# Optimization experiments

Hardware: AMD Instinct MI355X
Metric: run time of the kernel (lower is better)

## Reference

```python
import jax, jax.numpy as jnp
import numpy as np
import math

EMBED_DIM = 1024
NUM_HEADS = 16
HEAD_DIM = EMBED_DIM // NUM_HEADS
ROPE_BASE = 10000.0


def _rope_cache(seq_len, dim, dtype=jnp.float32):
    inv_freq = 1.0 / (ROPE_BASE ** (jnp.arange(0, dim, 2, dtype=jnp.float32) / dim))
    t = jnp.arange(seq_len, dtype=jnp.float32)
    freqs = t[:, None] * inv_freq[None, :]          # [S, D/2]
    emb = jnp.concatenate([freqs, freqs], axis=-1)  # [S, D]
    return jnp.cos(emb).astype(dtype), jnp.sin(emb).astype(dtype)


def _rotate_half(x):
    x1, x2 = jnp.split(x, 2, axis=-1)
    return jnp.concatenate([-x2, x1], axis=-1)


def setup_inputs() -> dict:
    key = jax.random.key(0)
    ks = jax.random.split(key, 12)
    B, S, E = 2, 2048, EMBED_DIM
    s = 1.0 / math.sqrt(E)
    inp = {
        "query": jax.random.normal(ks[0], (B, S, E), jnp.float32),
        "key": jax.random.normal(ks[1], (B, S, E), jnp.float32),
        "value": jax.random.normal(ks[2], (B, S, E), jnp.float32),
        "Wq": jax.random.normal(ks[3], (E, E), jnp.float32) * s,
        "bq": jnp.zeros((E,), jnp.float32),
        "Wk": jax.random.normal(ks[4], (E, E), jnp.float32) * s,
        "bk": jnp.zeros((E,), jnp.float32),
        "Wv": jax.random.normal(ks[5], (E, E), jnp.float32) * s,
        "bv": jnp.zeros((E,), jnp.float32),
        "Wo": jax.random.normal(ks[6], (E, E), jnp.float32) * s,
        "bo": jnp.zeros((E,), jnp.float32),
    }
    return inp


def reference(query, key, value, Wq, bq, Wk, bk, Wv, bv, Wo, bo):
    B, S, E = query.shape
    H, D = NUM_HEADS, HEAD_DIM

    def proj(x, W, b):  # torch Linear: x @ W.T + b -> [B,H,S,D]
        return (x @ W.T + b).reshape(B, -1, H, D).transpose(0, 2, 1, 3)

    q = proj(query, Wq, bq)
    k = proj(key, Wk, bk)
    v = proj(value, Wv, bv)

    cos, sin = _rope_cache(S, D, q.dtype)  # [S, D]
    cos = cos[None, None]                  # [1,1,S,D]
    sin = sin[None, None]
    q = q * cos + _rotate_half(q) * sin
    k = k * cos + _rotate_half(k) * sin

    scale = 1.0 / math.sqrt(D)
    scores = jnp.einsum("bhsd,bhtd->bhst", q, k) * scale  # [B,H,S,S]
    causal = jnp.triu(jnp.ones((S, S), bool), k=1)
    scores = jnp.where(causal[None, None], -jnp.inf, scores)
    attn = jax.nn.softmax(scores, axis=-1)
    out = jnp.einsum("bhst,bhtd->bhsd", attn, v)           # [B,H,S,D]
    out = out.transpose(0, 2, 1, 3).reshape(B, S, E)
    return out @ Wo.T + bo
```

## Files before the change

kernel.cpp:

```cpp
#include <hip/hip_runtime.h>
#include <math.h>

typedef unsigned short u16;
typedef __attribute__((ext_vector_type(4))) float f32x4;
typedef __attribute__((ext_vector_type(8))) short bf16x8;

#define SEQ   2048
#define EMB   1024
#define NH    16
#define HD    64
#define MROWS 4096

__device__ __forceinline__ u16 f2b(float f) {
    unsigned u = __float_as_uint(f);
    u += 0x7fff + ((u >> 16) & 1);
    return (u16)(u >> 16);
}
__device__ __forceinline__ unsigned pack_bf16x2(float a, float b) {
    unsigned ua = __float_as_uint(a) + 0x8000u;
    unsigned ub = __float_as_uint(b) + 0x8000u;
    return __builtin_amdgcn_perm(ub, ua, 0x07060302u);
}
__device__ __forceinline__ void gld16(const u16* g, const u16* l) {
    __builtin_amdgcn_global_load_lds((const __attribute__((address_space(1))) void*)g,
                                     (__attribute__((address_space(3))) void*)l, 16, 0, 0);
}

struct F2BArgs { const float* s[7]; u16* d[7]; };

__global__ void k_f2b(F2BArgs a) {
    int id = blockIdx.x;
    const float* src; u16* dst; int base;
    if (id < 6144) {
        int z = id >> 11;
        src = a.s[z]; dst = a.d[z];
        base = (id & 2047) << 8;
    } else {
        int r = id - 6144;
        int z = 3 + (r >> 9);
        src = a.s[z]; dst = a.d[z];
        base = (r & 511) << 8;
    }
    int i = base + threadIdx.x;
    const float4* s4 = (const float4*)src;
    float4 x = s4[i * 2], y = s4[i * 2 + 1];
    union { u16 u[8]; uint4 v; } o;
    o.u[0] = f2b(x.x); o.u[1] = f2b(x.y); o.u[2] = f2b(x.z); o.u[3] = f2b(x.w);
    o.u[4] = f2b(y.x); o.u[5] = f2b(y.y); o.u[6] = f2b(y.z); o.u[7] = f2b(y.w);
    ((uint4*)dst)[i] = o.v;
}

struct GemmArgs {
    const u16* A; const u16* Bw; const float* bias; u16* Cb;
};

__global__ __launch_bounds__(256) void k_gemm_qkv(GemmArgs g0, GemmArgs g1, GemmArgs g2) {
    __shared__ u16 sbuf[2][8192];

    int id = blockIdx.x;
    int x = id / 96;
    int rem = id % 96;
    int z = rem >> 5;
    int y = rem & 31;
    GemmArgs g = (z == 0) ? g0 : (z == 1 ? g1 : g2);

    int tid = threadIdx.x;
    int wave = tid >> 6, lane = tid & 63, quad = lane >> 4, l16 = lane & 15;
    int wm = wave >> 1, wn = wave & 1;
    int m0 = y * 128, n0 = x * 128;
    const int K = EMB;

    auto stage = [&](int k0, u16* buf) {
#pragma unroll
        for (int pp = 0; pp < 4; pp++) {
            int slot = pp * 256 + tid;
            int p = slot & 3;
            const u16* gsrc;
            if (pp < 2) {
                int row = slot >> 2;
                int c = p ^ (row & 3);
                gsrc = g.A + (size_t)(m0 + row) * K + k0 + c * 8;
            } else {
                int row = (slot >> 2) - 128;
                int c = p ^ (row & 3);
                gsrc = g.Bw + (size_t)(n0 + row) * K + k0 + c * 8;
            }
            gld16(gsrc, buf + slot * 8);
        }
    };

    f32x4 acc[4][4];
#pragma unroll
    for (int i = 0; i < 4; i++)
#pragma unroll
        for (int j = 0; j < 4; j++) acc[i][j] = (f32x4){0.f, 0.f, 0.f, 0.f};

    int nk = K >> 5;
    stage(0, sbuf[0]);
    for (int ks = 0; ks < nk; ks++) {
        __syncthreads();
        if (ks + 1 < nk) stage((ks + 1) << 5, sbuf[(ks + 1) & 1]);
        const u16* Ab = sbuf[ks & 1];
        const u16* Bb = Ab + 4096;
        bf16x8 af[4], bfr[4];
#pragma unroll
        for (int i = 0; i < 4; i++) {
            int row = wm * 64 + i * 16 + l16;
            af[i] = *(const bf16x8*)&Ab[row * 32 + (quad ^ (row & 3)) * 8];
        }
#pragma unroll
        for (int j = 0; j < 4; j++) {
            int row = wn * 64 + j * 16 + l16;
            bfr[j] = *(const bf16x8*)&Bb[row * 32 + (quad ^ (row & 3)) * 8];
        }
#pragma unroll
        for (int i = 0; i < 4; i++)
#pragma unroll
            for (int j = 0; j < 4; j++)
                acc[i][j] = __builtin_amdgcn_mfma_f32_16x16x32_bf16(af[i], bfr[j], acc[i][j], 0, 0, 0);
    }

    if (z < 2) {
        float qscale = (z == 0) ? 0.18033688011112042f : 1.0f;
#pragma unroll
        for (int j = 0; j < 2; j++) {
            int col1 = n0 + wn * 64 + j * 16 + l16;
            int dd1 = col1 & 63;
            int h = col1 >> 6;
            float inv = __expf(-(float)dd1 * 0.28782313662425575f);
            float b1 = g.bias[col1], b2 = g.bias[col1 + 32];
#pragma unroll
            for (int i = 0; i < 4; i++)
#pragma unroll
                for (int r = 0; r < 4; r++) {
                    int row = m0 + wm * 64 + i * 16 + quad * 4 + r;
                    int b = row >> 11, s = row & (SEQ - 1);
                    float sn, cs;
                    __sincosf((float)s * inv, &sn, &cs);
                    float x1 = acc[i][j][r] + b1;
                    float x2 = acc[i][j + 2][r] + b2;
                    size_t base = ((size_t)(b * NH + h) * SEQ + s) << 6;
                    g.Cb[base + dd1]      = f2b((x1 * cs - x2 * sn) * qscale);
                    g.Cb[base + dd1 + 32] = f2b((x2 * cs + x1 * sn) * qscale);
                }
        }
    } else {
        __syncthreads();
        u16* tr = &sbuf[0][0] + wave * 4096;
        int h = (n0 >> 6) + wn;
        int b = m0 >> 11;
        int s0 = (m0 & (SEQ - 1)) + wm * 64;
#pragma unroll
        for (int j = 0; j < 4; j++) {
            float bv = g.bias[n0 + wn * 64 + j * 16 + l16];
#pragma unroll
            for (int i = 0; i < 4; i++) {
                uint2 pk;
                pk.x = pack_bf16x2(acc[i][j][0] + bv, acc[i][j][1] + bv);
                pk.y = pack_bf16x2(acc[i][j][2] + bv, acc[i][j][3] + bv);
                int row = j * 16 + l16;
                int c4 = i * 4 + quad;
                *(uint2*)&tr[row * 64 + ((c4 ^ (row & 14)) << 2)] = pk;
            }
        }
        u16* dst = g.Cb + (((size_t)(b * NH + h) * HD) * SEQ) + s0;
#pragma unroll
        for (int ps = 0; ps < 8; ps++) {
            int d = ps * 8 + (lane >> 3);
            int c4 = (lane & 7) * 2;
            uint4 v = *(const uint4*)&tr[d * 64 + ((c4 ^ (d & 14)) << 2)];
            *(uint4*)&dst[(size_t)d * SEQ + c4 * 4] = v;
        }
    }
}

__global__ __launch_bounds__(256) void k_gemm_o(const u16* __restrict__ A,
                                                const u16* __restrict__ Bw,
                                                const float* __restrict__ bias,
                                                float* __restrict__ C) {
    __shared__ u16 sb[2][6144];
    int tid = threadIdx.x;
    int w = tid >> 6, lane = tid & 63, quad = lane >> 4, l16 = lane & 15;
    int y = blockIdx.x & 63, x = blockIdx.x >> 6;
    int m0 = y * 64, n0 = x * 128;
    const int K = EMB;

    auto stage = [&](int k0, u16* buf) {
#pragma unroll
        for (int pp = 0; pp < 3; pp++) {
            int slot = pp * 256 + tid;
            if (slot < 256) {
                int row = slot >> 2, p = slot & 3;
                int c = p ^ (row & 3);
                gld16(A + (size_t)(m0 + row) * K + k0 + c * 8, buf + slot * 8);
            } else {
                int s2 = slot - 256;
                int row = s2 >> 2, p = s2 & 3;
                int c = p ^ (row & 3);
                gld16(Bw + (size_t)(n0 + row) * K + k0 + c * 8, buf + 2048 + s2 * 8);
            }
        }
    };

    f32x4 acc[4][2];
#pragma unroll
    for (int i = 0; i < 4; i++)
#pragma unroll
        for (int j = 0; j < 2; j++) acc[i][j] = (f32x4){0.f, 0.f, 0.f, 0.f};

    int nk = K >> 5;
    stage(0, sb[0]);
    for (int ks = 0; ks < nk; ks++) {
        __syncthreads();
        if (ks + 1 < nk) stage((ks + 1) << 5, sb[(ks + 1) & 1]);
        const u16* Ab = sb[ks & 1];
        const u16* Bb = Ab + 2048;
        bf16x8 af[4], bf[2];
#pragma unroll
        for (int i = 0; i < 4; i++) {
            int row = i * 16 + l16;
            af[i] = *(const bf16x8*)&Ab[row * 32 + (quad ^ (row & 3)) * 8];
        }
#pragma unroll
        for (int j = 0; j < 2; j++) {
            int row = w * 32 + j * 16 + l16;
            bf[j] = *(const bf16x8*)&Bb[row * 32 + (quad ^ (row & 3)) * 8];
        }
#pragma unroll
        for (int i = 0; i < 4; i++)
#pragma unroll
            for (int j = 0; j < 2; j++)
                acc[i][j] = __builtin_amdgcn_mfma_f32_16x16x32_bf16(af[i], bf[j], acc[i][j], 0, 0, 0);
    }

#pragma unroll
    for (int i = 0; i < 4; i++)
#pragma unroll
        for (int r = 0; r < 4; r++) {
            int row = m0 + i * 16 + quad * 4 + r;
#pragma unroll
            for (int j = 0; j < 2; j++) {
                int col = n0 + w * 32 + j * 16 + l16;
                C[(size_t)row * EMB + col] = acc[i][j][r] + bias[col];
            }
        }
}

__global__ __launch_bounds__(512, 2) void k_attn(const u16* __restrict__ Q,
                                                 const u16* __restrict__ K,
                                                 const u16* __restrict__ Vt,
                                                 u16* __restrict__ O) {
    __shared__ u16 kv[4][8192];
    __shared__ u16 Pl[8][1024];
    int tid = threadIdx.x;
    int w = tid >> 6, lane = tid & 63, quad = lane >> 4, l16 = lane & 15;
    int pair = w & 3, par = w >> 2;
    int bh = blockIdx.x & 31;
    int qt = 15 - (blockIdx.x >> 5);
    int q0w = qt * 128 + pair * 32;

    const u16* Qb = Q + (size_t)bh * SEQ * HD;
    const u16* Kb = K + (size_t)bh * SEQ * HD;
    const u16* Vb = Vt + (size_t)bh * HD * SEQ;
    u16* pl = Pl[w];

    auto stage = [&](int t0, u16* buf) {
#pragma unroll
        for (int pp = 0; pp < 2; pp++) {
            int slot = pp * 512 + tid;
            int r = (slot >> 3) & 63;
            int p = slot & 7;
            int c = p ^ (r & 7);
            const u16* gsrc = (pp < 1) ? Kb + (size_t)(t0 + r) * HD + c * 8
                                       : Vb + (size_t)r * SEQ + t0 + c * 8;
            gld16(gsrc, buf + slot * 8);
        }
    };

    bf16x8 bq[2][2];
#pragma unroll
    for (int g = 0; g < 2; g++) {
        size_t base = (size_t)(q0w + g * 16 + l16) * HD + quad * 8;
        bq[g][0] = *(const bf16x8*)&Qb[base];
        bq[g][1] = *(const bf16x8*)&Qb[base + 32];
    }

    f32x4 o2[2][4];
#pragma unroll
    for (int g = 0; g < 2; g++)
#pragma unroll
        for (int jd = 0; jd < 4; jd++) o2[g][jd] = (f32x4){0.f, 0.f, 0.f, 0.f};
    float l_p[2] = {0.f, 0.f};

    int nsup = qt + 1;
    stage(0, kv[0]);
    stage(64, kv[2]);
    for (int k = 0; k < nsup; ++k) {
        __syncthreads();
        if (k + 1 < nsup) {
            stage((k + 1) * 128,      kv[(k + 1) & 1]);
            stage((k + 1) * 128 + 64, kv[2 + ((k + 1) & 1)]);
        }
        int t0 = k * 128 + par * 64;
        if (t0 > q0w + 31) continue;

        const u16* Kl = kv[par * 2 + (k & 1)];
        const u16* Vl = Kl + 4096;

        bf16x8 kf[4][2], vf[4][2];
#pragma unroll
        for (int mt = 0; mt < 4; mt++) {
            int row = mt * 16 + l16;
            kf[mt][0] = *(const bf16x8*)&Kl[row * 64 + (quad ^ (row & 7)) * 8];
            kf[mt][1] = *(const bf16x8*)&Kl[row * 64 + ((quad + 4) ^ (row & 7)) * 8];
            vf[mt][0] = *(const bf16x8*)&Vl[row * 64 + (quad ^ (row & 7)) * 8];
            vf[mt][1] = *(const bf16x8*)&Vl[row * 64 + ((quad + 4) ^ (row & 7)) * 8];
        }

#pragma unroll
        for (int g = 0; g < 2; g++) {
            int qmin = q0w + g * 16;
            if (t0 > qmin + 15) continue;

            f32x4 sc[4];
#pragma unroll
            for (int mt = 0; mt < 4; mt++) {
                sc[mt] = (f32x4){0.f, 0.f, 0.f, 0.f};
                sc[mt] = __builtin_amdgcn_mfma_f32_16x16x32_bf16(kf[mt][0], bq[g][0], sc[mt], 0, 0, 0);
                sc[mt] = __builtin_amdgcn_mfma_f32_16x16x32_bf16(kf[mt][1], bq[g][1], sc[mt], 0, 0, 0);
            }

            if (t0 + 63 > qmin) {
                int q = qmin + l16;
#pragma unroll
                for (int mt = 0; mt < 4; mt++)
#pragma unroll
                    for (int r = 0; r < 4; r++) {
                        int t = t0 + mt * 16 + quad * 4 + r;
                        if (t > q) sc[mt][r] = -INFINITY;
                    }
            }

            float rs = 0.f;
#pragma unroll
            for (int mt = 0; mt < 4; mt++)
#pragma unroll
                for (int r = 0; r < 4; r++) {
                    float p = __builtin_amdgcn_exp2f(sc[mt][r] - 64.f);
                    sc[mt][r] = p;
                    rs += p;
                }
            l_p[g] += rs;

#pragma unroll
            for (int mt = 0; mt < 4; mt++) {
                uint2 pk;
                pk.x = pack_bf16x2(sc[mt][0], sc[mt][1]);
                pk.y = pack_bf16x2(sc[mt][2], sc[mt][3]);
                int chunk = 2 * mt + (quad >> 1);
                *(uint2*)&pl[l16 * 64 + (chunk ^ (l16 & 7)) * 8 + (quad & 1) * 4] = pk;
            }

            bf16x8 pb0 = *(const bf16x8*)&pl[l16 * 64 + (quad ^ (l16 & 7)) * 8];
            bf16x8 pb1 = *(const bf16x8*)&pl[l16 * 64 + ((quad + 4) ^ (l16 & 7)) * 8];

#pragma unroll
            for (int jd = 0; jd < 4; jd++) {
                o2[g][jd] = __builtin_amdgcn_mfma_f32_16x16x32_bf16(vf[jd][0], pb0, o2[g][jd], 0, 0, 0);
                o2[g][jd] = __builtin_amdgcn_mfma_f32_16x16x32_bf16(vf[jd][1], pb1, o2[g][jd], 0, 0, 0);
            }
        }
    }

    __syncthreads();
    float* mp = (float*)&kv[0][0] + pair * 2176;
    if (par) {
#pragma unroll
        for (int g = 0; g < 2; g++) {
#pragma unroll
            for (int jd = 0; jd < 4; jd++)
                *(f32x4*)&mp[(g * 4 + jd) * 256 + lane * 4] = o2[g][jd];
            mp[2048 + g * 64 + lane] = l_p[g];
        }
    }
    __syncthreads();
    if (par) return;
#pragma unroll
    for (int g = 0; g < 2; g++) {
#pragma unroll
        for (int jd = 0; jd < 4; jd++)
            o2[g][jd] += *(const f32x4*)&mp[(g * 4 + jd) * 256 + lane * 4];
        l_p[g] += mp[2048 + g * 64 + lane];
    }

    u16* ep = ((u16*)&kv[0][0]) + 18432 + pair * 1216;
    int b = bh >> 4, h = bh & (NH - 1);
#pragma unroll
    for (int g = 0; g < 2; g++) {
        float l = l_p[g];
        l += __shfl_xor(l, 16, 64);
        l += __shfl_xor(l, 32, 64);
        float inv = 1.f / l;
#pragma unroll
        for (int jd = 0; jd < 4; jd++) {
            uint2 pk;
            pk.x = pack_bf16x2(o2[g][jd][0] * inv, o2[g][jd][1] * inv);
            pk.y = pack_bf16x2(o2[g][jd][2] * inv, o2[g][jd][3] * inv);
            *(uint2*)&ep[l16 * 72 + jd * 16 + quad * 4] = pk;
        }
        int row = lane >> 2, dc = (lane & 3) * 16;
        uint4 d0 = *(const uint4*)&ep[row * 72 + dc];
        uint4 d1 = *(const uint4*)&ep[row * 72 + dc + 8];
        int q = q0w + g * 16 + row;
        size_t addr = (size_t)(b * SEQ + q) * EMB + h * HD + dc;
        *(uint4*)&O[addr] = d0;
        *(uint4*)&O[addr + 8] = d1;
    }
}

extern "C" void kernel_launch(void* const* d_in, const int* in_sizes, int n_in,
                              void* d_out, int out_size, void* d_ws, size_t ws_size,
                              hipStream_t stream) {
    const float* query = (const float*)d_in[0];
    const float* key_  = (const float*)d_in[1];
    const float* value = (const float*)d_in[2];
    const float* Wq = (const float*)d_in[3];
    const float* bq = (const float*)d_in[4];
    const float* Wk = (const float*)d_in[5];
    const float* bk = (const float*)d_in[6];
    const float* Wv = (const float*)d_in[7];
    const float* bv = (const float*)d_in[8];
    const float* Wo = (const float*)d_in[9];
    const float* bo = (const float*)d_in[10];
    float* out = (float*)d_out;

    char* ws = (char*)d_ws;
    const size_t MB = 1u << 20;
    u16* xq  = (u16*)(ws + 0 * MB);
    u16* xk  = (u16*)(ws + 8 * MB);
    u16* xv  = (u16*)(ws + 16 * MB);
    u16* wqb = (u16*)(ws + 24 * MB);
    u16* wkb = (u16*)(ws + 26 * MB);
    u16* wvb = (u16*)(ws + 28 * MB);
    u16* wob = (u16*)(ws + 30 * MB);
    u16* Qp  = (u16*)(ws + 32 * MB);
    u16* Kp  = (u16*)(ws + 40 * MB);
    u16* Vt  = (u16*)(ws + 48 * MB);
    u16* Ab  = xk;

    F2BArgs fa;
    fa.s[0] = query; fa.s[1] = key_; fa.s[2] = value;
    fa.s[3] = Wq; fa.s[4] = Wk; fa.s[5] = Wv; fa.s[6] = Wo;
    fa.d[0] = xq; fa.d[1] = xk; fa.d[2] = xv;
    fa.d[3] = wqb; fa.d[4] = wkb; fa.d[5] = wvb; fa.d[6] = wob;
    k_f2b<<<8192, 256, 0, stream>>>(fa);

    GemmArgs gq = { xq, wqb, bq, Qp };
    GemmArgs gk = { xk, wkb, bk, Kp };
    GemmArgs gv = { xv, wvb, bv, Vt };
    k_gemm_qkv<<<768, 256, 0, stream>>>(gq, gk, gv);

    k_attn<<<512, 512, 0, stream>>>(Qp, Kp, Vt, Ab);

    k_gemm_o<<<512, 256, 0, stream>>>(Ab, wob, bo, out);
}
```

Before: 209.0 us.

## Enlarge QKV GEMM tile to 256x128 with triple-buffered async LDS pipeline

The QKV projection GEMM moves to 512-thread blocks, each computing a 256x128 tile, with a K-step of 64 and three LDS buffers kept two stages ahead. Waits use explicit vmcnt counts instead of __syncthreads, so global-to-LDS loads overlap with MFMA work, and the swizzle widens to 8 chunks for the 64-wide rows. The aim is to cut barrier and latency stalls and improve operand reuse. The cost is 144KB of LDS per block, which limits occupancy, and the hand-written waitcnt logic could be fragile.

```diff
diff --git a/kernel.cpp b/kernel.cpp
--- a/kernel.cpp
+++ b/kernel.cpp
@@ -54,35 +54,35 @@
     const u16* A; const u16* Bw; const float* bias; u16* Cb;
 };
 
-__global__ __launch_bounds__(256) void k_gemm_qkv(GemmArgs g0, GemmArgs g1, GemmArgs g2) {
-    __shared__ u16 sbuf[2][8192];
+__global__ __launch_bounds__(512, 2) void k_gemm_qkv(GemmArgs g0, GemmArgs g1, GemmArgs g2) {
+    __shared__ u16 sbuf[3][24576];
 
     int id = blockIdx.x;
-    int x = id / 96;
-    int rem = id % 96;
-    int z = rem >> 5;
-    int y = rem & 31;
+    int x = id / 48;
+    int rem = id % 48;
+    int z = rem >> 4;
+    int y = rem & 15;
     GemmArgs g = (z == 0) ? g0 : (z == 1 ? g1 : g2);
 
     int tid = threadIdx.x;
     int wave = tid >> 6, lane = tid & 63, quad = lane >> 4, l16 = lane & 15;
     int wm = wave >> 1, wn = wave & 1;
-    int m0 = y * 128, n0 = x * 128;
+    int m0 = y * 256, n0 = x * 128;
     const int K = EMB;
 
     auto stage = [&](int k0, u16* buf) {
 #pragma unroll
-        for (int pp = 0; pp < 4; pp++) {
-            int slot = pp * 256 + tid;
-            int p = slot & 3;
+        for (int pp = 0; pp < 6; pp++) {
+            int slot = pp * 512 + tid;
             const u16* gsrc;
-            if (pp < 2) {
-                int row = slot >> 2;
-                int c = p ^ (row & 3);
+            if (pp < 4) {
+                int row = slot >> 3, p = slot & 7;
+                int c = p ^ (row & 7);
                 gsrc = g.A + (size_t)(m0 + row) * K + k0 + c * 8;
             } else {
-                int row = (slot >> 2) - 128;
-                int c = p ^ (row & 3);
+                int s2 = slot - 2048;
+                int row = s2 >> 3, p = s2 & 7;
+                int c = p ^ (row & 7);
                 gsrc = g.Bw + (size_t)(n0 + row) * K + k0 + c * 8;
             }
             gld16(gsrc, buf + slot * 8);
@@ -95,29 +95,36 @@
 #pragma unroll
         for (int j = 0; j < 4; j++) acc[i][j] = (f32x4){0.f, 0.f, 0.f, 0.f};
 
-    int nk = K >> 5;
-    stage(0, sbuf[0]);
-    for (int ks = 0; ks < nk; ks++) {
-        __syncthreads();
-        if (ks + 1 < nk) stage((ks + 1) << 5, sbuf[(ks + 1) & 1]);
-        const u16* Ab = sbuf[ks & 1];
-        const u16* Bb = Ab + 4096;
-        bf16x8 af[4], bfr[4];
-#pragma unroll
-        for (int i = 0; i < 4; i++) {
-            int row = wm * 64 + i * 16 + l16;
-            af[i] = *(const bf16x8*)&Ab[row * 32 + (quad ^ (row & 3)) * 8];
-        }
-#pragma unroll
-        for (int j = 0; j < 4; j++) {
-            int row = wn * 64 + j * 16 + l16;
-            bfr[j] = *(const bf16x8*)&Bb[row * 32 + (quad ^ (row & 3)) * 8];
-        }
-#pragma unroll
-        for (int i = 0; i < 4; i++)
-#pragma unroll
-            for (int j = 0; j < 4; j++)
-                acc[i][j] = __builtin_amdgcn_mfma_f32_16x16x32_bf16(af[i], bfr[j], acc[i][j], 0, 0, 0);
+    int nt = K >> 6;
+    stage(0, &sbuf[0][0]);
+    stage(64, &sbuf[1][0]);
+    for (int t = 0; t < nt; ++t) {
+        if (t < nt - 1) asm volatile("s_waitcnt vmcnt(6)" ::: "memory");
+        else            asm volatile("s_waitcnt vmcnt(0)" ::: "memory");
+        asm volatile("s_barrier" ::: "memory");
+        if (t + 2 < nt) stage((t + 2) << 6, &sbuf[0][0] + ((t + 2) % 3) * 24576);
+
+        const u16* Ab = &sbuf[0][0] + (t % 3) * 24576;
+        const u16* Bb = Ab + 16384;
+#pragma unroll
+        for (int kk = 0; kk < 2; kk++) {
+            bf16x8 af[4], bfr[4];
+#pragma unroll
+            for (int i = 0; i < 4; i++) {
+                int row = wm * 64 + i * 16 + l16;
+                af[i] = *(const bf16x8*)&Ab[row * 64 + (((kk << 2) | quad) ^ (row & 7)) * 8];
+            }
+#pragma unroll
+            for (int j = 0; j < 4; j++) {
+                int row = wn * 64 + j * 16 + l16;
+                bfr[j] = *(const bf16x8*)&Bb[row * 64 + (((kk << 2) | quad) ^ (row & 7)) * 8];
+            }
+#pragma unroll
+            for (int i = 0; i < 4; i++)
+#pragma unroll
+                for (int j = 0; j < 4; j++)
+                    acc[i][j] = __builtin_amdgcn_mfma_f32_16x16x32_bf16(af[i], bfr[j], acc[i][j], 0, 0, 0);
+        }
     }
 
     if (z < 2) {
@@ -458,7 +465,7 @@
     GemmArgs gq = { xq, wqb, bq, Qp };
     GemmArgs gk = { xk, wkb, bk, Kp };
     GemmArgs gv = { xv, wvb, bv, Vt };
-    k_gemm_qkv<<<768, 256, 0, stream>>>(gq, gk, gv);
+    k_gemm_qkv<<<384, 512, 0, stream>>>(gq, gk, gv);
 
     k_attn<<<512, 512, 0, stream>>>(Qp, Kp, Vt, Ab);
 
```

New measurement: 205.3 us. About the same (-1.8%).
